# Optimization experiments

Measured on AMD Instinct MI355X. Metric: run time of the kernel, lower is better.

## Reference

```python
import jax, jax.numpy as jnp
import numpy as np

B, N, IN_DIM, OUT_DIM = 16, 2048, 512, 512

def _xavier(key, shape):
    bound = float(np.sqrt(6.0 / (shape[0] + shape[1])))
    return jax.random.uniform(key, shape, jnp.float32, -bound, bound)

def setup_inputs() -> dict:
    key = jax.random.key(0)
    kx, kk, kq, kv = jax.random.split(key, 4)
    return {
        "x": jax.random.normal(kx, (B, N, IN_DIM), jnp.float32),
        "W_key": _xavier(kk, (IN_DIM, OUT_DIM)),
        "W_query": _xavier(kq, (IN_DIM, OUT_DIM)),
        "W_value": _xavier(kv, (IN_DIM, OUT_DIM)),
    }

def reference(x, W_key, W_query, W_value):
    # projections: [B, N, out_dim]
    k = jnp.matmul(x, W_key)
    q = jnp.matmul(x, W_query)
    v = jnp.matmul(x, W_value)
    scale = jnp.sqrt(jnp.asarray(IN_DIM, jnp.float32))
    scores = jnp.einsum("bnd,bmd->bnm", q, k) / scale  # [B, N, N]
    weights = jax.nn.softmax(scores, axis=2)
    attn = jnp.einsum("bnm,bmd->bnd", weights, v)  # [B, N, out_dim]
    return jnp.mean(attn, axis=1)  # [B, out_dim]
```

## Files before the change

### kernel.cpp

```cpp
#include <hip/hip_runtime.h>
#include <hip/hip_bf16.h>
#include <hip/hip_fp16.h>
#include <stdint.h>

#define NB 16
#define NN 2048
#define ND 512
#define SSCALE 0.044194173824159216f

typedef unsigned short u16;
typedef unsigned int u32;
typedef float f32x4 __attribute__((ext_vector_type(4)));
typedef __bf16 bf16x8 __attribute__((ext_vector_type(8)));
typedef unsigned short u16x8 __attribute__((ext_vector_type(8)));

__device__ __forceinline__ float bf2f(u16 h) {
  union { u32 u; float f; } v; v.u = ((u32)h) << 16; return v.f;
}
__device__ __forceinline__ u16 f2bf(float f) {
  union { float f; u32 u; } v; v.f = f;
  u32 r = v.u + 0x7fffu + ((v.u >> 16) & 1u);
  return (u16)(r >> 16);
}
__device__ __forceinline__ u16 f2h(float f) {
  __half h = __float2half(f);
  union { __half h; u16 u; } v; v.h = h; return v.u;
}

__device__ __forceinline__ void async16(const void* g, void* l) {
  __builtin_amdgcn_global_load_lds(
      (const __attribute__((address_space(1))) u32*)g,
      (__attribute__((address_space(3))) u32*)l,
      16, 0, 0);
}

template <int MODE, bool AF32>
__global__ __launch_bounds__(256, 2) void gemm_bt(
    const void* __restrict__ Av, const u16* __restrict__ B, u16* __restrict__ C,
    float* __restrict__ Lrow, int lda, int ldb, int ldc, int K,
    long long sA, long long sB, long long sC, float cscale) {
  const int tid  = threadIdx.x;
  const int w    = tid >> 6;
  const int lane = tid & 63;
  const int wm   = w >> 1, wn = w & 1;
  const int lrow = lane & 15, quad = lane >> 4;
  const long long z = blockIdx.z;

  const float* Abf = (const float*)Av + z * sA + (size_t)blockIdx.y * 128 * lda;
  const u16*   Abh = (const u16*)Av   + z * sA + (size_t)blockIdx.y * 128 * lda;
  const u16*   Bb  = B + z * sB + (size_t)blockIdx.x * 128 * ldb;

  __shared__ __align__(16) u16 lds_a[128 * 32];
  __shared__ __align__(16) u16 lds_b[128 * 32];

  f32x4 acc[4][4];
#pragma unroll
  for (int i = 0; i < 4; i++)
#pragma unroll
    for (int j = 0; j < 4; j++) acc[i][j] = (f32x4){0.f, 0.f, 0.f, 0.f};

  for (int k0 = 0; k0 < K; k0 += 32) {
    if (k0) __syncthreads();
    if (AF32) {
      u16x8 va[2];
#pragma unroll
      for (int t = 0; t < 2; t++) {
        int ch  = t * 256 + tid;
        int row = ch >> 2;
        int cc  = (ch & 3) * 8;
        const float4* p = (const float4*)(Abf + (size_t)row * lda + k0 + cc);
        float4 f0 = p[0], f1 = p[1];
        u16x8 r;
        r[0] = f2bf(f0.x); r[1] = f2bf(f0.y); r[2] = f2bf(f0.z); r[3] = f2bf(f0.w);
        r[4] = f2bf(f1.x); r[5] = f2bf(f1.y); r[6] = f2bf(f1.z); r[7] = f2bf(f1.w);
        va[t] = r;
        async16(Bb + (size_t)row * ldb + k0 + cc, &lds_b[ch * 8]);
      }
#pragma unroll
      for (int t = 0; t < 2; t++) *(u16x8*)&lds_a[(t * 256 + tid) * 8] = va[t];
    } else {
#pragma unroll
      for (int t = 0; t < 2; t++) {
        int ch  = t * 256 + tid;
        int row = ch >> 2;
        int cc  = (ch & 3) * 8;
        async16(Abh + (size_t)row * lda + k0 + cc, &lds_a[ch * 8]);
        async16(Bb  + (size_t)row * ldb + k0 + cc, &lds_b[ch * 8]);
      }
    }
    __syncthreads();

    bf16x8 af[4], bfr[4];
#pragma unroll
    for (int i = 0; i < 4; i++) {
      af[i]  = *(const bf16x8*)&lds_a[(wm * 64 + i * 16 + lrow) * 32 + quad * 8];
      bfr[i] = *(const bf16x8*)&lds_b[(wn * 64 + i * 16 + lrow) * 32 + quad * 8];
    }
#pragma unroll
    for (int i = 0; i < 4; i++)
#pragma unroll
      for (int j = 0; j < 4; j++)
        acc[i][j] =
            __builtin_amdgcn_mfma_f32_16x16x32_bf16(af[i], bfr[j], acc[i][j], 0, 0, 0);
  }

  u16* Cb = C + z * sC + (size_t)blockIdx.y * 128 * ldc + (size_t)blockIdx.x * 128;
  if (MODE == 0) {
#pragma unroll
    for (int i = 0; i < 4; i++)
#pragma unroll
      for (int j = 0; j < 4; j++)
#pragma unroll
        for (int r = 0; r < 4; r++) {
          int row = wm * 64 + i * 16 + quad * 4 + r;
          int col = wn * 64 + j * 16 + lrow;
          Cb[(size_t)row * ldc + col] = f2bf(acc[i][j][r] * cscale);
        }
  } else {
    float* Lb = Lrow + z * NN + (size_t)blockIdx.y * 128;
#pragma unroll
    for (int i = 0; i < 4; i++)
#pragma unroll
      for (int r = 0; r < 4; r++) {
        int row = wm * 64 + i * 16 + quad * 4 + r;
        float rs = 0.f;
#pragma unroll
        for (int j = 0; j < 4; j++) {
          int col = wn * 64 + j * 16 + lrow;
          float e = __expf(fminf(acc[i][j][r] * cscale, 10.f));
          Cb[(size_t)row * ldc + col] = f2h(e);
          rs += e;
        }
        rs += __shfl_xor(rs, 1); rs += __shfl_xor(rs, 2);
        rs += __shfl_xor(rs, 4); rs += __shfl_xor(rs, 8);
        if (lrow == 0) atomicAdd(&Lb[row], rs);
      }
  }
}

__device__ __forceinline__ void stage_half(const u16* __restrict__ g, int ld,
                                           int row0, int k0,
                                           u16* __restrict__ l, int tid) {
  int r  = tid >> 3;
  int Lc = (tid & 7) ^ (r & 7);
  async16(g + (size_t)(row0 + r) * ld + k0 + Lc * 8, l + tid * 8);
  async16(g + (size_t)(row0 + 64 + r) * ld + k0 + Lc * 8, l + 4096 + tid * 8);
}

__device__ __forceinline__ bf16x8 ldf(const u16* __restrict__ h, int rbase,
                                      int lrow, int quad, int ks) {
  int rr = rbase + lrow;
  int pc = (ks * 4 + quad) ^ (lrow & 7);
  return *(const bf16x8*)&h[rr * 64 + pc * 8];
}

#define BAR() __builtin_amdgcn_s_barrier()
#define WAIT_LGKM()                                          \
  do {                                                       \
    asm volatile("s_waitcnt lgkmcnt(0)" ::: "memory");       \
    __builtin_amdgcn_sched_barrier(0);                       \
  } while (0)

#define READ_A(p, mh)                                                        \
  _Pragma("unroll") for (int i2 = 0; i2 < 4; ++i2)                           \
  _Pragma("unroll") for (int ks = 0; ks < 2; ++ks)                           \
      af[i2][ks] = ldf(sm + (p) * 32768 + wm * 8192, ((mh)*4 + i2) * 16,     \
                       lrow, quad, ks);

#define READ_B(p, nh)                                                        \
  _Pragma("unroll") for (int j2 = 0; j2 < 2; ++j2)                           \
  _Pragma("unroll") for (int ks = 0; ks < 2; ++ks)                           \
      bq[(nh)*2 + j2][ks] =                                                  \
          ldf(sm + (p) * 32768 + 16384 + (wn >> 1) * 8192,                   \
              (wn & 1) * 64 + ((nh)*2 + j2) * 16, lrow, quad, ks);

#define MFMA_Q(mh, nh)                                                       \
  __builtin_amdgcn_s_setprio(1);                                             \
  _Pragma("unroll") for (int i2 = 0; i2 < 4; ++i2)                           \
  _Pragma("unroll") for (int j2 = 0; j2 < 2; ++j2)                           \
  _Pragma("unroll") for (int ks = 0; ks < 2; ++ks)                           \
      acc[(mh)*4 + i2][(nh)*2 + j2] = __builtin_amdgcn_mfma_f32_16x16x32_bf16( \
          af[i2][ks], bq[(nh)*2 + j2][ks], acc[(mh)*4 + i2][(nh)*2 + j2],    \
          0, 0, 0);                                                          \
  __builtin_amdgcn_s_setprio(0);

#define STAGE_A(p, h, kt) \
  stage_half(Ab, lda, (h)*128, (kt)*64, sm + (p)*32768 + (h)*8192, tid)
#define STAGE_B(p, h, kt) \
  stage_half(Bb, ldb, (h)*128, (kt)*64, sm + (p)*32768 + 16384 + (h)*8192, tid)

template <int MODE>
__global__ __launch_bounds__(512, 2) void gemm256(
    const u16* __restrict__ A, const u16* __restrict__ B, u16* __restrict__ C,
    float* __restrict__ Lrow, int lda, int ldb, int ldc, int K,
    long long sA, long long sB, long long sC, float cscale) {
  const int tid  = threadIdx.x;
  const int wid  = tid >> 6, lane = tid & 63;
  const int wm   = wid >> 2, wn = wid & 3;
  const int lrow = lane & 15, quad = lane >> 4;

  const int ngx = gridDim.x, ngy = gridDim.y;
  int h   = blockIdx.x + ngx * (blockIdx.y + ngy * blockIdx.z);
  int nwg = ngx * ngy * (int)gridDim.z;
  int l   = (nwg & 7) ? h : ((h & 7) * (nwg >> 3) + (h >> 3));
  const int bxx = l % ngx;
  const int t2q = l / ngx;
  const int byy = t2q % ngy;
  const long long z = t2q / ngy;

  const u16* Ab = A + z * sA + (size_t)byy * 256 * lda;
  const u16* Bb = B + z * sB + (size_t)bxx * 256 * ldb;

  __shared__ __align__(16) u16 sm[65536];

  f32x4 acc[8][4];
#pragma unroll
  for (int i = 0; i < 8; i++)
#pragma unroll
    for (int j = 0; j < 4; j++) acc[i][j] = (f32x4){0.f, 0.f, 0.f, 0.f};

  bf16x8 af[4][2];
  bf16x8 bq[4][2];

  const int NITER = K >> 7;

  STAGE_A(0, 0, 0); STAGE_A(0, 1, 0);
  STAGE_B(0, 0, 0); STAGE_B(0, 1, 0);
  STAGE_B(1, 0, 1); STAGE_B(1, 1, 1);
  asm volatile("s_waitcnt vmcnt(4)" ::: "memory");
  __builtin_amdgcn_sched_barrier(0);
  BAR();

  for (int it = 0; it < NITER; ++it) {
    const int t = 2 * it;
    const bool more = (it + 1 < NITER);

    READ_A(0, 0); READ_B(0, 0);
    STAGE_A(1, 0, t + 1);
    BAR(); WAIT_LGKM();
    MFMA_Q(0, 0);
    BAR();
    READ_B(0, 1);
    STAGE_A(1, 1, t + 1);
    BAR(); WAIT_LGKM();
    MFMA_Q(0, 1);
    BAR();
    READ_A(0, 1);
    if (more) STAGE_B(0, 0, t + 2);
    BAR(); WAIT_LGKM();
    MFMA_Q(1, 0);
    BAR();
    if (more) STAGE_B(0, 1, t + 2);
    BAR();
    MFMA_Q(1, 1);
    if (more) { asm volatile("s_waitcnt vmcnt(4)" ::: "memory"); }
    else      { asm volatile("s_waitcnt vmcnt(0)" ::: "memory"); }
    __builtin_amdgcn_sched_barrier(0);
    BAR();
    READ_A(1, 0); READ_B(1, 0);
    if (more) STAGE_A(0, 0, t + 2);
    BAR(); WAIT_LGKM();
    MFMA_Q(0, 0);
    BAR();
    READ_B(1, 1);
    if (more) STAGE_A(0, 1, t + 2);
    BAR(); WAIT_LGKM();
    MFMA_Q(0, 1);
    BAR();
    READ_A(1, 1);
    if (more) STAGE_B(1, 0, t + 3);
    BAR(); WAIT_LGKM();
    MFMA_Q(1, 0);
    BAR();
    if (more) STAGE_B(1, 1, t + 3);
    BAR();
    MFMA_Q(1, 1);
    if (more) {
      asm volatile("s_waitcnt vmcnt(4)" ::: "memory");
      __builtin_amdgcn_sched_barrier(0);
    }
    BAR();
  }

  u16* Cb = C + z * sC +
            (size_t)(byy * 256 + wm * 128) * ldc +
            (size_t)bxx * 256 + wn * 64;
  if (MODE == 0) {
#pragma unroll
    for (int i = 0; i < 8; i++)
#pragma unroll
      for (int j = 0; j < 4; j++)
#pragma unroll
        for (int r = 0; r < 4; r++) {
          int row = i * 16 + quad * 4 + r;
          int col = j * 16 + lrow;
          Cb[(size_t)row * ldc + col] = f2bf(acc[i][j][r] * cscale);
        }
  } else {
    float* Lb = Lrow + z * NN + (size_t)byy * 256 + wm * 128;
#pragma unroll
    for (int i = 0; i < 8; i++)
#pragma unroll
      for (int r = 0; r < 4; r++) {
        int row = i * 16 + quad * 4 + r;
        float rs = 0.f;
#pragma unroll
        for (int j = 0; j < 4; j++) {
          int col = j * 16 + lrow;
          float e = __expf(fminf(acc[i][j][r] * cscale, 10.f));
          Cb[(size_t)row * ldc + col] = f2h(e);
          rs += e;
        }
        rs += __shfl_xor(rs, 1); rs += __shfl_xor(rs, 2);
        rs += __shfl_xor(rs, 4); rs += __shfl_xor(rs, 8);
        if (lrow == 0) atomicAdd(&Lb[row], rs);
      }
  }
}

__global__ void cast_f32_bf16(const float* __restrict__ x, u16* __restrict__ xb) {
  size_t i = ((size_t)blockIdx.x * 256 + threadIdx.x) * 8;
  float4 f0 = *(const float4*)(x + i);
  float4 f1 = *(const float4*)(x + i + 4);
  u16x8 r;
  r[0] = f2bf(f0.x); r[1] = f2bf(f0.y); r[2] = f2bf(f0.z); r[3] = f2bf(f0.w);
  r[4] = f2bf(f1.x); r[5] = f2bf(f1.y); r[6] = f2bf(f1.z); r[7] = f2bf(f1.w);
  *(u16x8*)(xb + i) = r;
}

__global__ void col_sum(const __half* __restrict__ E, const float* __restrict__ L,
                        float* __restrict__ c) {
  int m2 = blockIdx.x * 256 + threadIdx.x;
  int n0 = blockIdx.y * 128;
  int z  = blockIdx.z;
  const __half2* Ep = (const __half2*)(E + ((size_t)z * NN + n0) * NN) + m2;
  const float* lp = L + (size_t)z * NN + n0;
  float a0 = 0.f, a1 = 0.f;
#pragma unroll 4
  for (int n = 0; n < 128; n++) {
    __half2 h = Ep[(size_t)n * (NN / 2)];
    float il = 1.0f / lp[n];
    a0 += __low2float(h) * il;
    a1 += __high2float(h) * il;
  }
  atomicAdd(&c[(size_t)z * NN + m2 * 2], a0);
  atomicAdd(&c[(size_t)z * NN + m2 * 2 + 1], a1);
}

__global__ void tx_accum(const u16* __restrict__ xb, const float* __restrict__ c,
                         float* __restrict__ t) {
  int b = blockIdx.x, mc = blockIdx.y, d = threadIdx.x;
  const u16* vp = xb + ((size_t)b * NN + mc * 128) * ND;
  const float* cp = c + b * NN + mc * 128;
  float a0 = 0.f, a1 = 0.f;
#pragma unroll 4
  for (int m = 0; m < 128; m++) {
    float cm = cp[m];
    a0 += cm * bf2f(vp[(size_t)m * ND + d]);
    a1 += cm * bf2f(vp[(size_t)m * ND + 256 + d]);
  }
  atomicAdd(&t[b * ND + d], a0);
  atomicAdd(&t[b * ND + 256 + d], a1);
}

__global__ void final_wv(const float* __restrict__ t, const float* __restrict__ Wv,
                         float* __restrict__ out) {
  int b = blockIdx.x, d = blockIdx.y * 256 + threadIdx.x;
  const float* tb = t + b * ND;
  float a = 0.f;
#pragma unroll 4
  for (int l = 0; l < ND; l++) a += tb[l] * Wv[(size_t)l * ND + d];
  out[b * ND + d] = a * (1.f / (float)NN);
}

extern "C" void kernel_launch(void* const* d_in, const int* in_sizes, int n_in,
                              void* d_out, int out_size, void* d_ws, size_t ws_size,
                              hipStream_t stream) {
  const float* x  = (const float*)d_in[0];
  const float* Wk = (const float*)d_in[1];
  const float* Wq = (const float*)d_in[2];
  const float* Wv = (const float*)d_in[3];
  float* out = (float*)d_out;

  char* ws = (char*)d_ws;
  size_t off = 0;
  float* L   = (float*)(ws + off); off += (size_t)NB * NN * 4;
  float* c   = (float*)(ws + off); off += (size_t)NB * NN * 4;
  float* t   = (float*)(ws + off); off += (size_t)NB * ND * 4;
  u16* Wqb   = (u16*)(ws + off);   off += (size_t)ND * ND * 2;
  u16* Mt    = (u16*)(ws + off);   off += (size_t)ND * ND * 2;
  const size_t small_total = off;

  const size_t XBSZ = (size_t)NB * NN * ND * 2;
  const size_t SB1  = (size_t)NN * NN * 2;
  u16* xb   = (u16*)(ws + small_total);
  u16* y    = (u16*)(ws + small_total + XBSZ);
  __half* E = (__half*)(ws + small_total + 2 * XBSZ);
  size_t srem = ws_size > small_total + 2 * XBSZ
              ? ws_size - small_total - 2 * XBSZ : 0;
  int chb = 0, sr = 128;
  if      (srem >= 16 * SB1) chb = 16;
  else if (srem >=  8 * SB1) chb = 8;
  else if (srem >=  4 * SB1) chb = 4;
  else if (srem >=  2 * SB1) chb = 2;
  else if (srem >=  1 * SB1) chb = 1;
  else {
    if      (srem >= (size_t)1024 * NN * 2) sr = 1024;
    else if (srem >= (size_t)512  * NN * 2) sr = 512;
    else if (srem >= (size_t)256  * NN * 2) sr = 256;
  }

  hipMemsetAsync(L, 0, (size_t)(2 * NB * NN + NB * ND) * sizeof(float), stream);

  cast_f32_bf16<<<8192, 256, 0, stream>>>(x, xb);
  cast_f32_bf16<<<128, 256, 0, stream>>>(Wq, Wqb);

  gemm_bt<0, true><<<dim3(4, 4, 1), 256, 0, stream>>>(
      Wk, Wqb, Mt, nullptr, ND, ND, ND, ND, 0, 0, 0, SSCALE);

  gemm256<0><<<dim3(2, 128, 1), 512, 0, stream>>>(
      xb, Mt, y, nullptr, ND, ND, ND, ND, 0, 0, 0, 1.0f);

  const long long sR = (long long)NN * ND;
  const long long sS = (long long)NN * NN;

  if (chb >= 1) {
    for (int cc = 0; cc < NB / chb; ++cc) {
      size_t o = (size_t)cc * chb * NN;
      gemm256<1><<<dim3(8, 8, chb), 512, 0, stream>>>(
          y + o * ND, xb + o * ND, (u16*)E, L + o, ND, ND, NN, ND,
          sR, sR, sS, 1.0f);
      col_sum<<<dim3(4, 16, chb), 256, 0, stream>>>(E, L + o, c + o);
    }
  } else if (sr >= 256) {
    for (int b = 0; b < NB; ++b) {
      for (int ch = 0; ch < NN / sr; ++ch) {
        size_t o = (size_t)b * NN + (size_t)ch * sr;
        gemm256<1><<<dim3(8, sr / 256, 1), 512, 0, stream>>>(
            y + o * ND, xb + (size_t)b * NN * ND, (u16*)E, L + o,
            ND, ND, NN, ND, 0, 0, 0, 1.0f);
        col_sum<<<dim3(4, sr / 128, 1), 256, 0, stream>>>(E, L + o, c + b * NN);
      }
    }
  } else {
    for (int b = 0; b < NB; ++b) {
      for (int ch = 0; ch < NN / sr; ++ch) {
        size_t o = (size_t)b * NN + (size_t)ch * sr;
        gemm_bt<1, false><<<dim3(16, sr / 128, 1), 256, 0, stream>>>(
            y + o * ND, xb + (size_t)b * NN * ND, (u16*)E, L + o,
            ND, ND, NN, ND, 0, 0, 0, 1.0f);
        col_sum<<<dim3(4, sr / 128, 1), 256, 0, stream>>>(E, L + o, c + b * NN);
      }
    }
  }

  tx_accum<<<dim3(NB, 16), 256, 0, stream>>>(xb, c, t);
  final_wv<<<dim3(NB, 2), 256, 0, stream>>>(t, Wv, out);
  (void)in_sizes; (void)n_in; (void)out_size;
}
```

Measured before the change: 361.2 us.

## Recompute score GEMM twice instead of materializing exp matrix

The fp16 exp(score) matrix is no longer written to workspace and read back by col_sum. A first GEMM pass computes only the row sums L. A second pass recomputes the scores, normalizes them by 1/L and reduces the column sums directly into c with shuffles and atomics. This trades a large write-plus-read of the NxN matrix per batch for a second full score GEMM. It also drops the XCD-aware block remapping in gemm256 and the chunking logic that depended on workspace size.

```diff
diff --git a/kernel.cpp b/kernel.cpp
--- a/kernel.cpp
+++ b/kernel.cpp
@@ -21,10 +21,6 @@
   union { float f; u32 u; } v; v.f = f;
   u32 r = v.u + 0x7fffu + ((v.u >> 16) & 1u);
   return (u16)(r >> 16);
-}
-__device__ __forceinline__ u16 f2h(float f) {
-  __half h = __float2half(f);
-  union { __half h; u16 u; } v; v.h = h; return v.u;
 }
 
 __device__ __forceinline__ void async16(const void* g, void* l) {
@@ -105,37 +101,17 @@
   }
 
   u16* Cb = C + z * sC + (size_t)blockIdx.y * 128 * ldc + (size_t)blockIdx.x * 128;
-  if (MODE == 0) {
-#pragma unroll
-    for (int i = 0; i < 4; i++)
-#pragma unroll
-      for (int j = 0; j < 4; j++)
-#pragma unroll
-        for (int r = 0; r < 4; r++) {
-          int row = wm * 64 + i * 16 + quad * 4 + r;
-          int col = wn * 64 + j * 16 + lrow;
-          Cb[(size_t)row * ldc + col] = f2bf(acc[i][j][r] * cscale);
-        }
-  } else {
-    float* Lb = Lrow + z * NN + (size_t)blockIdx.y * 128;
-#pragma unroll
-    for (int i = 0; i < 4; i++)
+#pragma unroll
+  for (int i = 0; i < 4; i++)
+#pragma unroll
+    for (int j = 0; j < 4; j++)
 #pragma unroll
       for (int r = 0; r < 4; r++) {
         int row = wm * 64 + i * 16 + quad * 4 + r;
-        float rs = 0.f;
-#pragma unroll
-        for (int j = 0; j < 4; j++) {
-          int col = wn * 64 + j * 16 + lrow;
-          float e = __expf(fminf(acc[i][j][r] * cscale, 10.f));
-          Cb[(size_t)row * ldc + col] = f2h(e);
-          rs += e;
-        }
-        rs += __shfl_xor(rs, 1); rs += __shfl_xor(rs, 2);
-        rs += __shfl_xor(rs, 4); rs += __shfl_xor(rs, 8);
-        if (lrow == 0) atomicAdd(&Lb[row], rs);
-      }
-  }
+        int col = wn * 64 + j * 16 + lrow;
+        Cb[(size_t)row * ldc + col] = f2bf(acc[i][j][r] * cscale);
+      }
+  (void)Lrow;
 }
 
 __device__ __forceinline__ void stage_half(const u16* __restrict__ g, int ld,
@@ -192,21 +168,17 @@
 template <int MODE>
 __global__ __launch_bounds__(512, 2) void gemm256(
     const u16* __restrict__ A, const u16* __restrict__ B, u16* __restrict__ C,
-    float* __restrict__ Lrow, int lda, int ldb, int ldc, int K,
+    float* __restrict__ Lrow, float* __restrict__ Cacc,
+    int lda, int ldb, int ldc, int K,
     long long sA, long long sB, long long sC, float cscale) {
   const int tid  = threadIdx.x;
   const int wid  = tid >> 6, lane = tid & 63;
   const int wm   = wid >> 2, wn = wid & 3;
   const int lrow = lane & 15, quad = lane >> 4;
 
-  const int ngx = gridDim.x, ngy = gridDim.y;
-  int h   = blockIdx.x + ngx * (blockIdx.y + ngy * blockIdx.z);
-  int nwg = ngx * ngy * (int)gridDim.z;
-  int l   = (nwg & 7) ? h : ((h & 7) * (nwg >> 3) + (h >> 3));
-  const int bxx = l % ngx;
-  const int t2q = l / ngx;
-  const int byy = t2q % ngy;
-  const long long z = t2q / ngy;
+  const int bxx = blockIdx.x;
+  const int byy = blockIdx.y;
+  const long long z = blockIdx.z;
 
   const u16* Ab = A + z * sA + (size_t)byy * 256 * lda;
   const u16* Bb = B + z * sB + (size_t)bxx * 256 * ldb;
@@ -282,10 +254,10 @@
     BAR();
   }
 
-  u16* Cb = C + z * sC +
-            (size_t)(byy * 256 + wm * 128) * ldc +
-            (size_t)bxx * 256 + wn * 64;
   if (MODE == 0) {
+    u16* Cb = C + z * sC +
+              (size_t)(byy * 256 + wm * 128) * ldc +
+              (size_t)bxx * 256 + wn * 64;
 #pragma unroll
     for (int i = 0; i < 8; i++)
 #pragma unroll
@@ -296,25 +268,40 @@
           int col = j * 16 + lrow;
           Cb[(size_t)row * ldc + col] = f2bf(acc[i][j][r] * cscale);
         }
-  } else {
+  } else if (MODE == 1) {
     float* Lb = Lrow + z * NN + (size_t)byy * 256 + wm * 128;
 #pragma unroll
     for (int i = 0; i < 8; i++)
 #pragma unroll
       for (int r = 0; r < 4; r++) {
-        int row = i * 16 + quad * 4 + r;
         float rs = 0.f;
 #pragma unroll
-        for (int j = 0; j < 4; j++) {
-          int col = j * 16 + lrow;
-          float e = __expf(fminf(acc[i][j][r] * cscale, 10.f));
-          Cb[(size_t)row * ldc + col] = f2h(e);
-          rs += e;
-        }
+        for (int j = 0; j < 4; j++)
+          rs += __expf(fminf(acc[i][j][r] * cscale, 10.f));
         rs += __shfl_xor(rs, 1); rs += __shfl_xor(rs, 2);
         rs += __shfl_xor(rs, 4); rs += __shfl_xor(rs, 8);
-        if (lrow == 0) atomicAdd(&Lb[row], rs);
-      }
+        if (lrow == 0) atomicAdd(&Lb[i * 16 + quad * 4 + r], rs);
+      }
+  } else {
+    const float* Lb = Lrow + z * NN + (size_t)byy * 256 + wm * 128;
+    float* cb = Cacc + z * NN + (size_t)bxx * 256 + wn * 64;
+    float ca[4] = {0.f, 0.f, 0.f, 0.f};
+#pragma unroll
+    for (int i = 0; i < 8; i++)
+#pragma unroll
+      for (int r = 0; r < 4; r++) {
+        float il = 1.0f / Lb[i * 16 + quad * 4 + r];
+#pragma unroll
+        for (int j = 0; j < 4; j++)
+          ca[j] += __expf(fminf(acc[i][j][r] * cscale, 10.f)) * il;
+      }
+#pragma unroll
+    for (int j = 0; j < 4; j++) {
+      float v = ca[j];
+      v += __shfl_xor(v, 16);
+      v += __shfl_xor(v, 32);
+      if (quad == 0) atomicAdd(&cb[j * 16 + lrow], v);
+    }
   }
 }
 
@@ -326,25 +313,6 @@
   r[0] = f2bf(f0.x); r[1] = f2bf(f0.y); r[2] = f2bf(f0.z); r[3] = f2bf(f0.w);
   r[4] = f2bf(f1.x); r[5] = f2bf(f1.y); r[6] = f2bf(f1.z); r[7] = f2bf(f1.w);
   *(u16x8*)(xb + i) = r;
-}
-
-__global__ void col_sum(const __half* __restrict__ E, const float* __restrict__ L,
-                        float* __restrict__ c) {
-  int m2 = blockIdx.x * 256 + threadIdx.x;
-  int n0 = blockIdx.y * 128;
-  int z  = blockIdx.z;
-  const __half2* Ep = (const __half2*)(E + ((size_t)z * NN + n0) * NN) + m2;
-  const float* lp = L + (size_t)z * NN + n0;
-  float a0 = 0.f, a1 = 0.f;
-#pragma unroll 4
-  for (int n = 0; n < 128; n++) {
-    __half2 h = Ep[(size_t)n * (NN / 2)];
-    float il = 1.0f / lp[n];
-    a0 += __low2float(h) * il;
-    a1 += __high2float(h) * il;
-  }
-  atomicAdd(&c[(size_t)z * NN + m2 * 2], a0);
-  atomicAdd(&c[(size_t)z * NN + m2 * 2 + 1], a1);
 }
 
 __global__ void tx_accum(const u16* __restrict__ xb, const float* __restrict__ c,
@@ -389,26 +357,9 @@
   float* t   = (float*)(ws + off); off += (size_t)NB * ND * 4;
   u16* Wqb   = (u16*)(ws + off);   off += (size_t)ND * ND * 2;
   u16* Mt    = (u16*)(ws + off);   off += (size_t)ND * ND * 2;
-  const size_t small_total = off;
-
   const size_t XBSZ = (size_t)NB * NN * ND * 2;
-  const size_t SB1  = (size_t)NN * NN * 2;
-  u16* xb   = (u16*)(ws + small_total);
-  u16* y    = (u16*)(ws + small_total + XBSZ);
-  __half* E = (__half*)(ws + small_total + 2 * XBSZ);
-  size_t srem = ws_size > small_total + 2 * XBSZ
-              ? ws_size - small_total - 2 * XBSZ : 0;
-  int chb = 0, sr = 128;
-  if      (srem >= 16 * SB1) chb = 16;
-  else if (srem >=  8 * SB1) chb = 8;
-  else if (srem >=  4 * SB1) chb = 4;
-  else if (srem >=  2 * SB1) chb = 2;
-  else if (srem >=  1 * SB1) chb = 1;
-  else {
-    if      (srem >= (size_t)1024 * NN * 2) sr = 1024;
-    else if (srem >= (size_t)512  * NN * 2) sr = 512;
-    else if (srem >= (size_t)256  * NN * 2) sr = 256;
-  }
+  u16* xb = (u16*)(ws + off);
+  u16* y  = (u16*)(ws + off + XBSZ);
 
   hipMemsetAsync(L, 0, (size_t)(2 * NB * NN + NB * ND) * sizeof(float), stream);
 
@@ -419,40 +370,15 @@
       Wk, Wqb, Mt, nullptr, ND, ND, ND, ND, 0, 0, 0, SSCALE);
 
   gemm256<0><<<dim3(2, 128, 1), 512, 0, stream>>>(
-      xb, Mt, y, nullptr, ND, ND, ND, ND, 0, 0, 0, 1.0f);
+      xb, Mt, y, nullptr, nullptr, ND, ND, ND, ND, 0, 0, 0, 1.0f);
 
   const long long sR = (long long)NN * ND;
-  const long long sS = (long long)NN * NN;
-
-  if (chb >= 1) {
-    for (int cc = 0; cc < NB / chb; ++cc) {
-      size_t o = (size_t)cc * chb * NN;
-      gemm256<1><<<dim3(8, 8, chb), 512, 0, stream>>>(
-          y + o * ND, xb + o * ND, (u16*)E, L + o, ND, ND, NN, ND,
-          sR, sR, sS, 1.0f);
-      col_sum<<<dim3(4, 16, chb), 256, 0, stream>>>(E, L + o, c + o);
-    }
-  } else if (sr >= 256) {
-    for (int b = 0; b < NB; ++b) {
-      for (int ch = 0; ch < NN / sr; ++ch) {
-        size_t o = (size_t)b * NN + (size_t)ch * sr;
-        gemm256<1><<<dim3(8, sr / 256, 1), 512, 0, stream>>>(
-            y + o * ND, xb + (size_t)b * NN * ND, (u16*)E, L + o,
-            ND, ND, NN, ND, 0, 0, 0, 1.0f);
-        col_sum<<<dim3(4, sr / 128, 1), 256, 0, stream>>>(E, L + o, c + b * NN);
-      }
-    }
-  } else {
-    for (int b = 0; b < NB; ++b) {
-      for (int ch = 0; ch < NN / sr; ++ch) {
-        size_t o = (size_t)b * NN + (size_t)ch * sr;
-        gemm_bt<1, false><<<dim3(16, sr / 128, 1), 256, 0, stream>>>(
-            y + o * ND, xb + (size_t)b * NN * ND, (u16*)E, L + o,
-            ND, ND, NN, ND, 0, 0, 0, 1.0f);
-        col_sum<<<dim3(4, sr / 128, 1), 256, 0, stream>>>(E, L + o, c + b * NN);
-      }
-    }
-  }
+
+  gemm256<1><<<dim3(8, 8, NB), 512, 0, stream>>>(
+      y, xb, nullptr, L, nullptr, ND, ND, 0, ND, sR, sR, 0, 1.0f);
+
+  gemm256<2><<<dim3(8, 8, NB), 512, 0, stream>>>(
+      y, xb, nullptr, L, c, ND, ND, 0, ND, sR, sR, 0, 1.0f);
 
   tx_accum<<<dim3(NB, 16), 256, 0, stream>>>(xb, c, t);
   final_wv<<<dim3(NB, 2), 256, 0, stream>>>(t, Wv, out);
```

Result: slower. 378.1 us (+4.7%).
